# Optimization experiments

Measured on AMD Instinct MI355X. Metric: run time of the kernel, lower is better.

The kernel has to match this reference:

```python
import jax, jax.numpy as jnp
import numpy as np

HIDDEN = 1280
HEADS = 16
HEAD_DIM = HIDDEN // HEADS  # 80
TOTAL = 8192
N_CHUNKS = 8


def rotate_half(x):
    x1, x2 = jnp.split(x, 2, axis=-1)
    return jnp.concatenate([-x2, x1], axis=-1)


def setup_inputs() -> dict:
    key = jax.random.key(0)
    ks = jax.random.split(key, 7)
    hidden_states = jax.random.normal(ks[0], (TOTAL, HIDDEN), dtype=jnp.float32)
    cos = jax.random.uniform(ks[1], (TOTAL, HEAD_DIM), dtype=jnp.float32)
    sin = jax.random.uniform(ks[2], (TOTAL, HEAD_DIM), dtype=jnp.float32)
    s = 1.0 / np.sqrt(HIDDEN)
    w_qkv = jax.random.normal(ks[3], (HIDDEN, 3 * HIDDEN), dtype=jnp.float32) * s
    b_qkv = jax.random.normal(ks[4], (3 * HIDDEN,), dtype=jnp.float32) * 0.01
    w_proj = jax.random.normal(ks[5], (HIDDEN, HIDDEN), dtype=jnp.float32) * s
    b_proj = jax.random.normal(ks[6], (HIDDEN,), dtype=jnp.float32) * 0.01
    return {"hidden_states": hidden_states, "cos": cos, "sin": sin,
            "w_qkv": w_qkv, "b_qkv": b_qkv, "w_proj": w_proj,
            "b_proj": b_proj, "n_chunks": N_CHUNKS}


def reference(hidden_states, cos, sin, w_qkv, b_qkv, w_proj, b_proj, n_chunks):
    T, D = hidden_states.shape
    C = int(n_chunks)
    L = T // C  # equal-length chunks (block-diagonal varlen attention)
    H, hd = HEADS, HEAD_DIM
    scale = hd ** -0.5

    qkv = hidden_states @ w_qkv + b_qkv                    # [T, 3D]
    q, k, v = jnp.split(qkv, 3, axis=-1)
    # [C, L, H, hd]
    q = q.reshape(C, L, H, hd)
    k = k.reshape(C, L, H, hd)
    v = v.reshape(C, L, H, hd)
    cos_c = cos.reshape(C, L, 1, hd)
    sin_c = sin.reshape(C, L, 1, hd)
    q = q * cos_c + rotate_half(q) * sin_c
    k = k * cos_c + rotate_half(k) * sin_c

    # block-diagonal attention: each chunk attends only within itself
    scores = jnp.einsum('clhd,cmhd->chlm', q, k) * scale   # [C, H, L, L]
    weights = jax.nn.softmax(scores.astype(jnp.float32), axis=-1).astype(v.dtype)
    attn = jnp.einsum('chlm,cmhd->clhd', weights, v)       # [C, L, H, hd]
    attn = attn.reshape(T, D)
    return attn @ w_proj + b_proj
```

## Files before the change

### kernel.cpp

```cpp
#include <hip/hip_runtime.h>

#define T_TOK 8192
#define D_HID 1280
#define H_    16
#define HD_   80
#define C_    8
#define L_    1024
#define N3_   3840
#define QPAD  96

typedef _Float16 f16;
typedef __attribute__((ext_vector_type(8))) _Float16 h8;
typedef __attribute__((ext_vector_type(4))) float f32x4;

__global__ __launch_bounds__(256) void convert_x(const float* __restrict__ x,
                                                 f16* __restrict__ y) {
  const int g = blockIdx.x * 256 + threadIdx.x;
  const float4 v = ((const float4*)x)[g];
  f16 o[4] = {(f16)v.x, (f16)v.y, (f16)v.z, (f16)v.w};
  ((uint2*)y)[g] = *(const uint2*)o;
}

__global__ __launch_bounds__(256) void convert_w_t(const float* __restrict__ W,
                                                   f16* __restrict__ Wt,
                                                   int K, int N) {
  __shared__ float tile[32][33];
  const int n0 = blockIdx.x * 32, k0 = blockIdx.y * 32;
  const int c = threadIdx.x & 31, r0 = threadIdx.x >> 5;
#pragma unroll
  for (int it = 0; it < 4; ++it) {
    const int r = r0 + it * 8;
    tile[r][c] = W[(size_t)(k0 + r) * N + n0 + c];
  }
  __syncthreads();
#pragma unroll
  for (int it = 0; it < 4; ++it) {
    const int r = r0 + it * 8;
    Wt[(size_t)(n0 + r) * K + k0 + c] = (f16)tile[c][r];
  }
}

__device__ __forceinline__ void stage_half(const f16* __restrict__ gpanel, int K,
                                           f16* sdst, int t, int half) {
#pragma unroll
  for (int r = 0; r < 2; ++r) {
    const int s = r * 512 + (int)threadIdx.x;
    const int row = half * 128 + (s >> 3);
    const int part = (s & 7) ^ (row & 7);
    const f16* gp = gpanel + (size_t)row * K + t * 64 + part * 8;
    __builtin_amdgcn_global_load_lds(
        (const __attribute__((address_space(1))) void*)gp,
        (__attribute__((address_space(3))) void*)(sdst + row * 64 + (s & 7) * 8),
        16, 0, 0);
  }
}

__device__ __forceinline__ h8 fragld64(const f16* s, int row, int c) {
  const int slot = c ^ (row & 7);
  return *(const h8*)&s[row * 64 + slot * 8];
}

__global__ __launch_bounds__(512, 2) void gemm_f16(
    const f16* __restrict__ A, const f16* __restrict__ B,
    const float* __restrict__ bias,
    float* __restrict__ Cf, f16* __restrict__ Ch,
    int M, int N, int K) {
  __shared__ f16 sAB[2][2][256 * 64];
  const int tid = threadIdx.x;
  const int wave = tid >> 6, lane = tid & 63;
  const int quad = lane >> 4, ln = lane & 15;

  const int nwg = gridDim.x;
  int wg = blockIdx.x;
  wg = (wg & 7) * (nwg >> 3) + (wg >> 3);
  const int nbx = N >> 8;
  const int bm = (wg / nbx) * 256, bn = (wg % nbx) * 256;
  const int wm = (wave >> 2) * 128, wn = (wave & 3) * 64;

  f32x4 acc[8][4];
#pragma unroll
  for (int i = 0; i < 8; ++i)
#pragma unroll
    for (int j = 0; j < 4; ++j) acc[i][j] = (f32x4){0.f, 0.f, 0.f, 0.f};

  const f16* Abase = A + (size_t)bm * K;
  const f16* Bbase = B + (size_t)bn * K;
  const int nt = K >> 6;

  stage_half(Abase, K, sAB[0][0], 0, 0);
  stage_half(Abase, K, sAB[0][0], 0, 1);
  stage_half(Bbase, K, sAB[0][1], 0, 0);
  stage_half(Bbase, K, sAB[0][1], 0, 1);
  stage_half(Abase, K, sAB[1][0], 1, 0);
  stage_half(Abase, K, sAB[1][0], 1, 1);
  asm volatile("s_waitcnt vmcnt(4)" ::: "memory");
  __builtin_amdgcn_sched_barrier(0);
  __builtin_amdgcn_s_barrier();

  for (int t = 0; t < nt; ++t) {
    const f16* sA = sAB[t & 1][0];
    const f16* sB = sAB[t & 1][1];
    const int nb = (t + 1) & 1;
    h8 af[4][2], af2[4][2], bf01[2][2], bf23[2][2];

#pragma unroll
    for (int i = 0; i < 4; ++i)
#pragma unroll
      for (int ks = 0; ks < 2; ++ks)
        af[i][ks] = fragld64(sA, wm + i * 16 + ln, ks * 4 + quad);
#pragma unroll
    for (int j = 0; j < 2; ++j)
#pragma unroll
      for (int ks = 0; ks < 2; ++ks)
        bf01[j][ks] = fragld64(sB, wn + j * 16 + ln, ks * 4 + quad);
#pragma unroll
    for (int j = 0; j < 2; ++j)
#pragma unroll
      for (int ks = 0; ks < 2; ++ks)
        bf23[j][ks] = fragld64(sB, wn + (j + 2) * 16 + ln, ks * 4 + quad);
    if (t + 1 < nt) stage_half(Bbase, K, sAB[nb][1], t + 1, 0);

    __builtin_amdgcn_s_setprio(1);
#pragma unroll
    for (int ks = 0; ks < 2; ++ks)
#pragma unroll
      for (int i = 0; i < 4; ++i)
#pragma unroll
        for (int j = 0; j < 2; ++j)
          acc[i][j] = __builtin_amdgcn_mfma_f32_16x16x32_f16(af[i][ks], bf01[j][ks], acc[i][j], 0, 0, 0);
    __builtin_amdgcn_s_setprio(0);

#pragma unroll
    for (int i = 0; i < 4; ++i)
#pragma unroll
      for (int ks = 0; ks < 2; ++ks)
        af2[i][ks] = fragld64(sA, wm + (i + 4) * 16 + ln, ks * 4 + quad);
    if (t + 1 < nt) stage_half(Bbase, K, sAB[nb][1], t + 1, 1);

    __builtin_amdgcn_s_setprio(1);
#pragma unroll
    for (int ks = 0; ks < 2; ++ks)
#pragma unroll
      for (int i = 0; i < 4; ++i)
#pragma unroll
        for (int j = 0; j < 2; ++j)
          acc[i][j + 2] = __builtin_amdgcn_mfma_f32_16x16x32_f16(af[i][ks], bf23[j][ks], acc[i][j + 2], 0, 0, 0);
    __builtin_amdgcn_s_setprio(0);

    asm volatile("s_waitcnt lgkmcnt(0)" ::: "memory");
    __builtin_amdgcn_sched_barrier(0);
    __builtin_amdgcn_s_barrier();
    if (t + 2 < nt) {
      stage_half(Abase, K, sAB[t & 1][0], t + 2, 0);
      stage_half(Abase, K, sAB[t & 1][0], t + 2, 1);
    }

    __builtin_amdgcn_s_setprio(1);
#pragma unroll
    for (int ks = 0; ks < 2; ++ks)
#pragma unroll
      for (int i = 0; i < 4; ++i)
#pragma unroll
        for (int j = 0; j < 2; ++j)
          acc[i + 4][j + 2] = __builtin_amdgcn_mfma_f32_16x16x32_f16(af2[i][ks], bf23[j][ks], acc[i + 4][j + 2], 0, 0, 0);
#pragma unroll
    for (int ks = 0; ks < 2; ++ks)
#pragma unroll
      for (int i = 0; i < 4; ++i)
#pragma unroll
        for (int j = 0; j < 2; ++j)
          acc[i + 4][j] = __builtin_amdgcn_mfma_f32_16x16x32_f16(af2[i][ks], bf01[j][ks], acc[i + 4][j], 0, 0, 0);
    __builtin_amdgcn_s_setprio(0);

    if (t + 1 < nt) {
      if (t + 2 < nt) asm volatile("s_waitcnt vmcnt(4)" ::: "memory");
      else            asm volatile("s_waitcnt vmcnt(0)" ::: "memory");
      __builtin_amdgcn_sched_barrier(0);
      __builtin_amdgcn_s_barrier();
    }
  }

  float bv[4];
#pragma unroll
  for (int j = 0; j < 4; ++j) bv[j] = bias[bn + wn + j * 16 + ln];
#pragma unroll
  for (int i = 0; i < 8; ++i)
#pragma unroll
    for (int j = 0; j < 4; ++j)
#pragma unroll
      for (int r = 0; r < 4; ++r) {
        const int row = bm + wm + i * 16 + quad * 4 + r;
        const int col = bn + wn + j * 16 + ln;
        const float val = acc[i][j][r] + bv[j];
        if (Ch) Ch[(size_t)row * N + col] = (f16)val;
        else    Cf[(size_t)row * N + col] = val;
      }
}

__global__ __launch_bounds__(256) void rope_convert(
    const f16* __restrict__ qkv, const float* __restrict__ cosb,
    const float* __restrict__ sinb, f16* __restrict__ Qb, f16* __restrict__ Kb) {
  const int tid = threadIdx.x;
  const int wave = tid >> 6, lane = tid & 63;
  const int t = blockIdx.x * 4 + wave;
  const size_t rowb = (size_t)t * N3_;
  const float qscale = 0.16129821086f;
#pragma unroll
  for (int u = 0; u < 5; ++u) {
    const int g = u * 64 + lane;
    const int e = g * 8;
    const int d = e % HD_;
    const int h = (e % D_HID) / HD_;
    const bool isK = e >= D_HID;
    const bool lo = d < 40;
    const int pe = lo ? e + 40 : e - 40;
    f16 v[8], p[8];
    *(int4*)v = *(const int4*)(qkv + rowb + e);
    *(int4*)p = *(const int4*)(qkv + rowb + pe);
    const float4 cs0 = *(const float4*)(cosb + (size_t)t * HD_ + d);
    const float4 cs1 = *(const float4*)(cosb + (size_t)t * HD_ + d + 4);
    const float4 sn0 = *(const float4*)(sinb + (size_t)t * HD_ + d);
    const float4 sn1 = *(const float4*)(sinb + (size_t)t * HD_ + d + 4);
    const float cs[8] = {cs0.x, cs0.y, cs0.z, cs0.w, cs1.x, cs1.y, cs1.z, cs1.w};
    const float sn[8] = {sn0.x, sn0.y, sn0.z, sn0.w, sn1.x, sn1.y, sn1.z, sn1.w};
    f16 o[8];
#pragma unroll
    for (int j = 0; j < 8; ++j) {
      const float pv = lo ? -(float)p[j] : (float)p[j];
      const float ov = (float)v[j] * cs[j] + pv * sn[j];
      o[j] = (f16)(isK ? ov : ov * qscale);
    }
    *(int4*)((isK ? Kb : Qb) + ((size_t)h * T_TOK + t) * QPAD + d) = *(const int4*)o;
  }
  {
    const int qk = lane >> 5, h = (lane >> 1) & 15, half = lane & 1;
    f16* dst = (qk ? Kb : Qb) + ((size_t)h * T_TOK + t) * QPAD + 80 + half * 8;
    *(int4*)dst = make_int4(0, 0, 0, 0);
  }
}

__global__ __launch_bounds__(256) void vt_convert(const f16* __restrict__ qkv,
                                                  f16* __restrict__ Vt) {
  __shared__ f16 tl[HD_][136];
  const int h = blockIdx.x & 15;
  const int t0 = (blockIdx.x >> 4) * 128;
  const int tid = threadIdx.x;
#pragma unroll
  for (int it = 0; it < 5; ++it) {
    const int e = tid + it * 256;
    const int t = e / 10, pc = e % 10;
    int4 v = *(const int4*)(qkv + (size_t)(t0 + t) * N3_ + 2 * D_HID + h * HD_ + pc * 8);
    f16 tmp[8];
    *(int4*)tmp = v;
#pragma unroll
    for (int u = 0; u < 8; ++u) tl[pc * 8 + u][t] = tmp[u];
  }
  __syncthreads();
#pragma unroll
  for (int it = 0; it < 5; ++it) {
    const int e = tid + it * 256;
    const int d = e >> 4, pt = e & 15;
    *(int4*)(Vt + ((size_t)h * HD_ + d) * T_TOK + t0 + pt * 8) = *(const int4*)&tl[d][pt * 8];
  }
}

__global__ __launch_bounds__(256, 2) void attn_flash(
    const f16* __restrict__ Qb, const f16* __restrict__ Kb,
    const f16* __restrict__ Vt, f16* __restrict__ Oa) {
  __shared__ f16 Ps[4][64][72];
  const int tid = threadIdx.x;
  const int wave = tid >> 6, lane = tid & 63;
  const int quad = lane >> 4, ln = lane & 15;
  const int h = blockIdx.x & 15;
  const int qb = (blockIdx.x >> 4) & 3;
  const int c = blockIdx.x >> 6;
  const int t0 = c * L_ + qb * 256 + wave * 64;
  const size_t hb = (size_t)h * T_TOK;

  h8 aq[4][3];
#pragma unroll
  for (int i = 0; i < 4; ++i)
#pragma unroll
    for (int ks = 0; ks < 3; ++ks)
      aq[i][ks] = *(const h8*)(Qb + (hb + t0 + i * 16 + ln) * QPAD + ks * 32 + quad * 8);

  f32x4 o[4][5];
  float lsum[4][4];
#pragma unroll
  for (int i = 0; i < 4; ++i) {
#pragma unroll
    for (int jn = 0; jn < 5; ++jn) o[i][jn] = (f32x4){0.f, 0.f, 0.f, 0.f};
#pragma unroll
    for (int r = 0; r < 4; ++r) lsum[i][r] = 0.f;
  }

  for (int kb = 0; kb < 16; ++kb) {
    const int kt0 = c * L_ + kb * 64;
#pragma unroll
    for (int j = 0; j < 4; ++j) {
      h8 bk[3];
#pragma unroll
      for (int ks = 0; ks < 3; ++ks)
        bk[ks] = *(const h8*)(Kb + (hb + kt0 + j * 16 + ln) * QPAD + ks * 32 + quad * 8);
      f32x4 s[4];
#pragma unroll
      for (int i = 0; i < 4; ++i) s[i] = (f32x4){0.f, 0.f, 0.f, 0.f};
      __builtin_amdgcn_s_setprio(1);
#pragma unroll
      for (int ks = 0; ks < 3; ++ks)
#pragma unroll
        for (int i = 0; i < 4; ++i)
          s[i] = __builtin_amdgcn_mfma_f32_16x16x32_f16(aq[i][ks], bk[ks], s[i], 0, 0, 0);
      __builtin_amdgcn_s_setprio(0);
#pragma unroll
      for (int i = 0; i < 4; ++i)
#pragma unroll
        for (int r = 0; r < 4; ++r) {
          const float p = exp2f(s[i][r]);
          lsum[i][r] += p;
          Ps[wave][i * 16 + quad * 4 + r][j * 16 + ln] = (f16)p;
        }
    }
#pragma unroll
    for (int ks = 0; ks < 2; ++ks) {
      h8 ap[4];
#pragma unroll
      for (int i = 0; i < 4; ++i)
        ap[i] = *(const h8*)&Ps[wave][i * 16 + ln][ks * 32 + quad * 8];
#pragma unroll
      for (int jn = 0; jn < 5; ++jn) {
        const h8 bv = *(const h8*)(Vt + ((size_t)h * HD_ + jn * 16 + ln) * T_TOK
                                   + kt0 + ks * 32 + quad * 8);
        __builtin_amdgcn_s_setprio(1);
#pragma unroll
        for (int i = 0; i < 4; ++i)
          o[i][jn] = __builtin_amdgcn_mfma_f32_16x16x32_f16(ap[i], bv, o[i][jn], 0, 0, 0);
        __builtin_amdgcn_s_setprio(0);
      }
    }
  }

#pragma unroll
  for (int i = 0; i < 4; ++i)
#pragma unroll
    for (int r = 0; r < 4; ++r) {
      float s = lsum[i][r];
#pragma unroll
      for (int off = 1; off < 16; off <<= 1) s += __shfl_xor(s, off);
      lsum[i][r] = 1.f / s;
    }

#pragma unroll
  for (int i = 0; i < 4; ++i)
#pragma unroll
    for (int r = 0; r < 4; ++r) {
      const int t = t0 + i * 16 + quad * 4 + r;
      const float inv = lsum[i][r];
#pragma unroll
      for (int jn = 0; jn < 5; ++jn)
        Oa[(size_t)t * D_HID + h * HD_ + jn * 16 + ln] = (f16)(o[i][jn][r] * inv);
    }
}

extern "C" void kernel_launch(void* const* d_in, const int* in_sizes, int n_in,
                              void* d_out, int out_size, void* d_ws, size_t ws_size,
                              hipStream_t stream) {
  (void)in_sizes; (void)n_in; (void)out_size; (void)ws_size;
  const float* x      = (const float*)d_in[0];
  const float* cosb   = (const float*)d_in[1];
  const float* sinb   = (const float*)d_in[2];
  const float* w_qkv  = (const float*)d_in[3];
  const float* b_qkv  = (const float*)d_in[4];
  const float* w_proj = (const float*)d_in[5];
  const float* b_proj = (const float*)d_in[6];
  float* out = (float*)d_out;

  char* ws = (char*)d_ws;
  f16* qkv_h  = (f16*)(ws);
  f16* attn_h = (f16*)(ws);
  f16* x_h    = (f16*)(ws + 62914560);
  f16* Qb     = (f16*)(ws + 62914560);
  f16* Kb     = (f16*)(ws + 88080384);
  f16* Vt     = (f16*)(ws + 113246208);
  f16* wq_t   = (f16*)(ws + 134217728);
  f16* wp_t   = (f16*)(ws + 144048128);

  convert_x<<<(T_TOK * D_HID / 4) / 256, 256, 0, stream>>>(x, x_h);
  convert_w_t<<<dim3(N3_ / 32, D_HID / 32), 256, 0, stream>>>(w_qkv, wq_t, D_HID, N3_);
  convert_w_t<<<dim3(D_HID / 32, D_HID / 32), 256, 0, stream>>>(w_proj, wp_t, D_HID, D_HID);
  gemm_f16<<<(N3_ / 256) * (T_TOK / 256), 512, 0, stream>>>(
      x_h, wq_t, b_qkv, nullptr, qkv_h, T_TOK, N3_, D_HID);
  rope_convert<<<T_TOK / 4, 256, 0, stream>>>(qkv_h, cosb, sinb, Qb, Kb);
  vt_convert<<<H_ * (T_TOK / 128), 256, 0, stream>>>(qkv_h, Vt);
  attn_flash<<<C_ * 4 * H_, 256, 0, stream>>>(Qb, Kb, Vt, attn_h);
  gemm_f16<<<(D_HID / 256) * (T_TOK / 256), 512, 0, stream>>>(
      attn_h, wp_t, b_proj, out, nullptr, T_TOK, D_HID, D_HID);
}
```

Before: 373.7 us.

## Split attention key range in two and combine partial outputs

The attention kernel now splits each chunk's key blocks into two halves and launches twice as many blocks. Each block writes an unnormalized fp16 partial output and its row sums. A new combine kernel adds the two partials and divides by the summed denominators. Launch bounds are raised to 4 blocks per CU to get more resident waves, at the cost of tighter register limits (possible spills), extra partial-output traffic and an extra kernel launch.

New measurement: 695.3 us. +86.1%, slower.

```diff
diff --git a/kernel.cpp b/kernel.cpp
--- a/kernel.cpp
+++ b/kernel.cpp
@@ -264,16 +264,17 @@
   }
 }
 
-__global__ __launch_bounds__(256, 2) void attn_flash(
+__global__ __launch_bounds__(256, 4) void attn_flash(
     const f16* __restrict__ Qb, const f16* __restrict__ Kb,
-    const f16* __restrict__ Vt, f16* __restrict__ Oa) {
+    const f16* __restrict__ Vt, f16* __restrict__ Op, float* __restrict__ Ls) {
   __shared__ f16 Ps[4][64][72];
   const int tid = threadIdx.x;
   const int wave = tid >> 6, lane = tid & 63;
   const int quad = lane >> 4, ln = lane & 15;
   const int h = blockIdx.x & 15;
   const int qb = (blockIdx.x >> 4) & 3;
-  const int c = blockIdx.x >> 6;
+  const int split = (blockIdx.x >> 6) & 1;
+  const int c = blockIdx.x >> 7;
   const int t0 = c * L_ + qb * 256 + wave * 64;
   const size_t hb = (size_t)h * T_TOK;
 
@@ -294,7 +295,7 @@
     for (int r = 0; r < 4; ++r) lsum[i][r] = 0.f;
   }
 
-  for (int kb = 0; kb < 16; ++kb) {
+  for (int kb = split * 8; kb < split * 8 + 8; ++kb) {
     const int kt0 = c * L_ + kb * 64;
 #pragma unroll
     for (int j = 0; j < 4; ++j) {
@@ -347,7 +348,7 @@
       float s = lsum[i][r];
 #pragma unroll
       for (int off = 1; off < 16; off <<= 1) s += __shfl_xor(s, off);
-      lsum[i][r] = 1.f / s;
+      lsum[i][r] = s;
     }
 
 #pragma unroll
@@ -355,11 +356,31 @@
 #pragma unroll
     for (int r = 0; r < 4; ++r) {
       const int t = t0 + i * 16 + quad * 4 + r;
-      const float inv = lsum[i][r];
 #pragma unroll
       for (int jn = 0; jn < 5; ++jn)
-        Oa[(size_t)t * D_HID + h * HD_ + jn * 16 + ln] = (f16)(o[i][jn][r] * inv);
-    }
+        Op[((size_t)split * T_TOK + t) * D_HID + h * HD_ + jn * 16 + ln] =
+            (f16)o[i][jn][r];
+      if (ln == 0)
+        Ls[(size_t)split * H_ * T_TOK + (size_t)h * T_TOK + t] = lsum[i][r];
+    }
+}
+
+__global__ __launch_bounds__(256) void attn_combine(
+    const f16* __restrict__ Op, const float* __restrict__ Ls,
+    f16* __restrict__ Oa) {
+  const size_t e = ((size_t)blockIdx.x * 256 + threadIdx.x) * 8;
+  const int t = (int)(e / D_HID), col = (int)(e % D_HID);
+  const int h = col / HD_;
+  f16 a[8], b[8], o[8];
+  *(int4*)a = *(const int4*)(Op + e);
+  *(int4*)b = *(const int4*)(Op + (size_t)T_TOK * D_HID + e);
+  const float l0 = Ls[(size_t)h * T_TOK + t];
+  const float l1 = Ls[(size_t)H_ * T_TOK + (size_t)h * T_TOK + t];
+  const float inv = 1.f / (l0 + l1);
+#pragma unroll
+  for (int j = 0; j < 8; ++j)
+    o[j] = (f16)(((float)a[j] + (float)b[j]) * inv);
+  *(int4*)(Oa + e) = *(const int4*)o;
 }
 
 extern "C" void kernel_launch(void* const* d_in, const int* in_sizes, int n_in,
@@ -377,12 +398,14 @@
 
   char* ws = (char*)d_ws;
   f16* qkv_h  = (f16*)(ws);
-  f16* attn_h = (f16*)(ws);
+  f16* Opart  = (f16*)(ws);
+  f16* attn_h = (f16*)(ws + 41943040);
   f16* x_h    = (f16*)(ws + 62914560);
   f16* Qb     = (f16*)(ws + 62914560);
   f16* Kb     = (f16*)(ws + 88080384);
   f16* Vt     = (f16*)(ws + 113246208);
   f16* wq_t   = (f16*)(ws + 134217728);
+  float* Ls   = (float*)(ws + 134217728);
   f16* wp_t   = (f16*)(ws + 144048128);
 
   convert_x<<<(T_TOK * D_HID / 4) / 256, 256, 0, stream>>>(x, x_h);
@@ -392,7 +415,8 @@
       x_h, wq_t, b_qkv, nullptr, qkv_h, T_TOK, N3_, D_HID);
   rope_convert<<<T_TOK / 4, 256, 0, stream>>>(qkv_h, cosb, sinb, Qb, Kb);
   vt_convert<<<H_ * (T_TOK / 128), 256, 0, stream>>>(qkv_h, Vt);
-  attn_flash<<<C_ * 4 * H_, 256, 0, stream>>>(Qb, Kb, Vt, attn_h);
+  attn_flash<<<C_ * 4 * H_ * 2, 256, 0, stream>>>(Qb, Kb, Vt, Opart, Ls);
+  attn_combine<<<(T_TOK * D_HID / 8) / 256, 256, 0, stream>>>(Opart, Ls, attn_h);
   gemm_f16<<<(D_HID / 256) * (T_TOK / 256), 512, 0, stream>>>(
       attn_h, wp_t, b_proj, out, nullptr, T_TOK, D_HID, D_HID);
 }
```
